# Optimization experiments

Measured on AMD Instinct MI355X. Metric: run time of the kernel, lower is better.

The kernel has to match this reference:

```python
import jax, jax.numpy as jnp
import numpy as np

DIM = 192
SCALE = DIM ** (-0.5)


def setup_inputs() -> dict:
    key = jax.random.key(0)
    qkv = jax.random.normal(key, (8, 4096, 3 * DIM), dtype=jnp.float32)
    return {"qkv": qkv}


def reference(qkv):
    # qkv: [B, T, 3C] -> q, k, v each [B, T, C]
    q, k, v = jnp.split(qkv, 3, axis=2)
    # scale_in=True: scale q and k before distance computation
    q = q * SCALE
    k = k * SCALE
    # L2-distance attention logits: -||q_t - k_s||_2, computed via the
    # expansion ||q||^2 + ||k||^2 - 2 q.k (same as torch.cdist for large inputs)
    q2 = jnp.sum(q * q, axis=-1)          # [B, T]
    k2 = jnp.sum(k * k, axis=-1)          # [B, S]
    d2 = q2[:, :, None] + k2[:, None, :] - 2.0 * jnp.einsum('btc,bsc->bts', q, k)
    d2 = jnp.maximum(d2, 0.0)
    # safe sqrt (zero distance on the diagonal since q and k come from same tokens)
    dist = jnp.where(d2 > 0, jnp.sqrt(jnp.where(d2 > 0, d2, 1.0)), 0.0)
    attn_logits = -dist                    # [B, T, S]
    attn = jax.nn.softmax(attn_logits, axis=-1)
    return jnp.einsum('bts,bsc->btc', attn, v)  # [B, T, C]
```

## Files before the change

kernel.cpp:

```cpp
#include <hip/hip_runtime.h>
#include <hip/hip_bf16.h>


#define BB 8
#define TT 4096
#define CD 192

typedef __attribute__((ext_vector_type(8))) short short8;
typedef __attribute__((ext_vector_type(4))) float float4v;
typedef __attribute__((ext_vector_type(2))) unsigned int uint2v;

constexpr float A2C = (float)(2.0813689810056077 / 192.0);

static __device__ __forceinline__ unsigned short f2bf(float f) {
  unsigned u = __builtin_bit_cast(unsigned, f);
  unsigned r = u + 0x7fffu + ((u >> 16) & 1u);
  return (unsigned short)(r >> 16);
}
static __device__ __forceinline__ float bf2f(unsigned short b) {
  return __builtin_bit_cast(float, (unsigned)b << 16);
}

__global__ __launch_bounds__(256) void prep(
    const float* __restrict__ qkv, short8* __restrict__ qsw,
    short8* __restrict__ ksw, short8* __restrict__ vsw,
    float* __restrict__ q2, float* __restrict__ k2) {
  __shared__ unsigned short tile[32 * 584];
  const int t = threadIdx.x;
  const int b = blockIdx.x >> 7;
  const int sc = blockIdx.x & 127;
  const float* src = qkv + ((size_t)(b * TT + sc * 32)) * (3 * CD);
#pragma unroll
  for (int j = 0; j < 18; ++j) {
    int f = j * 256 + t;
    int row = f / 144, c4 = (f % 144) * 4;
    float4v x = *(const float4v*)(src + (size_t)row * 576 + c4);
    unsigned r0 = (unsigned)f2bf(x[0]) | ((unsigned)f2bf(x[1]) << 16);
    unsigned r1 = (unsigned)f2bf(x[2]) | ((unsigned)f2bf(x[3]) << 16);
    *(uint2v*)&tile[row * 584 + c4] = (uint2v){r0, r1};
  }
  __syncthreads();

  const int lane = t & 63, w = t >> 6;
  const int L = lane & 15, q = lane >> 4;
  const int which = w >> 1;
  const int s16o = w & 1;
  const int row = s16o * 16 + L;
  short8* dst = which ? ksw : qsw;
  const size_t ubase = ((size_t)(b * 256 + sc * 2 + s16o)) * 6;
  float ss = 0.f;
#pragma unroll
  for (int ch = 0; ch < 6; ++ch) {
    short8 fr = *(const short8*)&tile[row * 584 + which * CD + ch * 32 + q * 8];
#pragma unroll
    for (int j = 0; j < 8; ++j) {
      float f = bf2f((unsigned short)fr[j]);
      ss += f * f;
    }
    dst[(ubase + ch) * 64 + lane] = fr;
  }
  ss += __shfl_xor(ss, 16);
  ss += __shfl_xor(ss, 32);
  if (lane < 16)
    (which ? k2 : q2)[b * TT + sc * 32 + s16o * 16 + lane] = ss * A2C;

#pragma unroll
  for (int i = 0; i < 3; ++i) {
    int nt2 = w * 3 + i;
    short8 fr;
#pragma unroll
    for (int j = 0; j < 8; ++j)
      fr[j] = (short)tile[(q * 8 + j) * 584 + 2 * CD + nt2 * 16 + L];
    vsw[((size_t)(b * 12 + nt2) * 128 + sc) * 64 + lane] = fr;
  }
}

__global__ __launch_bounds__(256, 2) void attn2(
    const short8* __restrict__ qsw, const short8* __restrict__ ksw,
    const short8* __restrict__ vsw, const float* __restrict__ q2,
    const float* __restrict__ k2, float* __restrict__ out) {
  __shared__ __align__(16) unsigned char s_lds[49152 + 9216];
  float* ldsP = (float*)(s_lds + 49152);

  const int tid = threadIdx.x;
  const int w = tid >> 6;
  const int lane = tid & 63;
  const int L = lane & 15;
  const int q = lane >> 4;
  const int b = blockIdx.x & 7;
  const int qt = blockIdx.x >> 3;
  const int q0 = qt * 64 + w * 16;
  const size_t bT = (size_t)b * TT;

  float* pw = ldsP + w * 576;

  auto stage = [&](int itile, int buf) {
    const char* gk = (const char*)(ksw + ((size_t)(b * 256 + 2 * itile)) * 6 * 64);
#pragma unroll
    for (int j = 0; j < 3; ++j) {
      int u = w * 3 + j;
      const char* ga = gk + (u * 64 + lane) * 16;
      char* la = (char*)s_lds + buf * 12288 + u * 1024;
      __builtin_amdgcn_global_load_lds(
          (const __attribute__((address_space(1))) void*)ga,
          (__attribute__((address_space(3))) void*)la, 16, 0, 0);
    }
#pragma unroll
    for (int j = 0; j < 3; ++j) {
      int u = w * 3 + j;
      const char* ga = (const char*)vsw +
                       (((size_t)(b * 12 + u) * 128 + itile) * 64 + lane) * 16;
      char* la = (char*)s_lds + 24576 + buf * 12288 + u * 1024;
      __builtin_amdgcn_global_load_lds(
          (const __attribute__((address_space(1))) void*)ga,
          (__attribute__((address_space(3))) void*)la, 16, 0, 0);
    }
  };

  short8 qf[6];
#pragma unroll
  for (int ch = 0; ch < 6; ++ch)
    qf[ch] = qsw[((size_t)(b * 256 + (q0 >> 4)) * 6 + ch) * 64 + lane];

  float q2l[4];
#pragma unroll
  for (int r = 0; r < 4; ++r) q2l[r] = q2[bT + q0 + 4 * q + r];

  float4v oacc[12];
#pragma unroll
  for (int nt = 0; nt < 12; ++nt) oacc[nt] = (float4v){0.f, 0.f, 0.f, 0.f};
  float lsum[4] = {0.f, 0.f, 0.f, 0.f};

  stage(0, 0);
  __syncthreads();

#pragma unroll 1
  for (int it = 0; it < 128; ++it) {
    const int cur = it & 1;
    if (it + 1 < 128) stage(it + 1, cur ^ 1);
    const int s0 = it * 32;

    float k2l[2];
    k2l[0] = k2[bT + s0 + L];
    k2l[1] = k2[bT + s0 + 16 + L];

    float4v sacc[2];
    sacc[0] = (float4v){0.f, 0.f, 0.f, 0.f};
    sacc[1] = (float4v){0.f, 0.f, 0.f, 0.f};
#pragma unroll
    for (int ch = 0; ch < 6; ++ch) {
      short8 kf0 = *(const short8*)(s_lds + cur * 12288 + ch * 1024 + lane * 16);
      short8 kf1 = *(const short8*)(s_lds + cur * 12288 + (6 + ch) * 1024 + lane * 16);
      sacc[0] = __builtin_amdgcn_mfma_f32_16x16x32_bf16(qf[ch], kf0, sacc[0], 0, 0, 0);
      sacc[1] = __builtin_amdgcn_mfma_f32_16x16x32_bf16(qf[ch], kf1, sacc[1], 0, 0, 0);
    }

    short8 vf[12];
#pragma unroll
    for (int nt = 0; nt < 12; ++nt)
      vf[nt] = *(const short8*)(s_lds + 24576 + cur * 12288 + nt * 1024 + lane * 16);

#pragma unroll
    for (int nt = 0; nt < 2; ++nt)
#pragma unroll
      for (int r = 0; r < 4; ++r) {
        float dot = sacc[nt][r];
        float tt = fmaf(-2.f * A2C, dot, q2l[r] + k2l[nt]);
        float y = fmaxf(tt, 0.f);
        float p = __builtin_amdgcn_exp2f(-__builtin_amdgcn_sqrtf(y));
        lsum[r] += p;
        pw[(4 * q + r) * 36 + nt * 16 + L] = p;
      }
    float4v p0 = *(const float4v*)(pw + L * 36 + q * 8);
    float4v p1 = *(const float4v*)(pw + L * 36 + q * 8 + 4);
    short8 paf;
#pragma unroll
    for (int j = 0; j < 4; ++j) {
      paf[j] = (short)f2bf(p0[j]);
      paf[j + 4] = (short)f2bf(p1[j]);
    }

#pragma unroll
    for (int nt = 0; nt < 12; ++nt)
      oacc[nt] = __builtin_amdgcn_mfma_f32_16x16x32_bf16(paf, vf[nt], oacc[nt], 0, 0, 0);

    __syncthreads();
  }

#pragma unroll
  for (int r = 0; r < 4; ++r) {
    float ls = lsum[r];
#pragma unroll
    for (int m = 1; m < 16; m <<= 1) ls += __shfl_xor(ls, m);
    float linv = 1.f / ls;
#pragma unroll
    for (int nt = 0; nt < 12; ++nt)
      out[(bT + q0 + 4 * q + r) * CD + nt * 16 + L] = oacc[nt][r] * linv;
  }
}

extern "C" void kernel_launch(void* const* d_in, const int* in_sizes, int n_in,
                              void* d_out, int out_size, void* d_ws, size_t ws_size,
                              hipStream_t stream) {
  (void)in_sizes; (void)n_in; (void)out_size; (void)ws_size;
  const float* qkv = (const float*)d_in[0];
  float* out = (float*)d_out;

  short8* qsw = (short8*)d_ws;
  short8* ksw = qsw + (size_t)BB * 256 * 6 * 64;
  short8* vsw = ksw + (size_t)BB * 256 * 6 * 64;
  float* q2 = (float*)(vsw + (size_t)BB * 12 * 128 * 64);
  float* k2 = q2 + (size_t)BB * TT;

  prep<<<BB * 128, 256, 0, stream>>>(qkv, qsw, ksw, vsw, q2, k2);
  attn2<<<BB * 64, 256, 0, stream>>>(qsw, ksw, vsw, q2, k2, out);
}
```

Measured before the change: 244.3 us.

## Switch to fp16, compute transposed scores in registers, split output channels across blocks

Converts Q/K/V staging from bf16 to fp16. Computes S^T (K as the A operand) so each lane's probabilities already sit in the layout the PV MFMA (16x16x16 f16) expects, which removes the LDS round trip through the P scratch buffer. Each wave now handles 32 query rows but only half of the 192 output channels, with a second block covering the other half. Per-block V staging and LDS usage shrink, at the cost of computing QK^T twice across the two channel-half blocks. The move to fp16 changes precision, and values outside the fp16 range could overflow.

Measured after the change: 299.7 us. +22.6%, slower.

```diff
diff --git a/kernel.cpp b/kernel.cpp
--- a/kernel.cpp
+++ b/kernel.cpp
@@ -6,25 +6,26 @@
 #define TT 4096
 #define CD 192
 
+typedef __attribute__((ext_vector_type(8))) _Float16 half8;
+typedef __attribute__((ext_vector_type(4))) _Float16 half4;
 typedef __attribute__((ext_vector_type(8))) short short8;
 typedef __attribute__((ext_vector_type(4))) float float4v;
 typedef __attribute__((ext_vector_type(2))) unsigned int uint2v;
 
 constexpr float A2C = (float)(2.0813689810056077 / 192.0);
-
-static __device__ __forceinline__ unsigned short f2bf(float f) {
-  unsigned u = __builtin_bit_cast(unsigned, f);
-  unsigned r = u + 0x7fffu + ((u >> 16) & 1u);
-  return (unsigned short)(r >> 16);
-}
-static __device__ __forceinline__ float bf2f(unsigned short b) {
-  return __builtin_bit_cast(float, (unsigned)b << 16);
+constexpr float M2A2C = -2.0f * A2C;
+
+static __device__ __forceinline__ unsigned short f2h(float f) {
+  return __builtin_bit_cast(unsigned short, (_Float16)f);
+}
+static __device__ __forceinline__ float h2f(unsigned short u) {
+  return (float)__builtin_bit_cast(_Float16, u);
 }
 
 __global__ __launch_bounds__(256) void prep(
     const float* __restrict__ qkv, short8* __restrict__ qsw,
     short8* __restrict__ ksw, short8* __restrict__ vsw,
-    float* __restrict__ q2, float* __restrict__ k2) {
+    float* __restrict__ q2A, float* __restrict__ k2A) {
   __shared__ unsigned short tile[32 * 584];
   const int t = threadIdx.x;
   const int b = blockIdx.x >> 7;
@@ -35,8 +36,8 @@
     int f = j * 256 + t;
     int row = f / 144, c4 = (f % 144) * 4;
     float4v x = *(const float4v*)(src + (size_t)row * 576 + c4);
-    unsigned r0 = (unsigned)f2bf(x[0]) | ((unsigned)f2bf(x[1]) << 16);
-    unsigned r1 = (unsigned)f2bf(x[2]) | ((unsigned)f2bf(x[3]) << 16);
+    unsigned r0 = (unsigned)f2h(x[0]) | ((unsigned)f2h(x[1]) << 16);
+    unsigned r1 = (unsigned)f2h(x[2]) | ((unsigned)f2h(x[3]) << 16);
     *(uint2v*)&tile[row * 584 + c4] = (uint2v){r0, r1};
   }
   __syncthreads();
@@ -54,7 +55,7 @@
     short8 fr = *(const short8*)&tile[row * 584 + which * CD + ch * 32 + q * 8];
 #pragma unroll
     for (int j = 0; j < 8; ++j) {
-      float f = bf2f((unsigned short)fr[j]);
+      float f = h2f((unsigned short)fr[j]);
       ss += f * f;
     }
     dst[(ubase + ch) * 64 + lane] = fr;
@@ -62,25 +63,26 @@
   ss += __shfl_xor(ss, 16);
   ss += __shfl_xor(ss, 32);
   if (lane < 16)
-    (which ? k2 : q2)[b * TT + sc * 32 + s16o * 16 + lane] = ss * A2C;
+    (which ? k2A : q2A)[b * TT + sc * 32 + s16o * 16 + lane] = ss * A2C;
 
 #pragma unroll
   for (int i = 0; i < 3; ++i) {
-    int nt2 = w * 3 + i;
+    int ct = w * 3 + i;
     short8 fr;
 #pragma unroll
-    for (int j = 0; j < 8; ++j)
-      fr[j] = (short)tile[(q * 8 + j) * 584 + 2 * CD + nt2 * 16 + L];
-    vsw[((size_t)(b * 12 + nt2) * 128 + sc) * 64 + lane] = fr;
-  }
-}
-
-__global__ __launch_bounds__(256, 2) void attn2(
+    for (int j = 0; j < 4; ++j) {
+      fr[j]     = (short)tile[(4 * q + j) * 584 + 2 * CD + ct * 16 + L];
+      fr[j + 4] = (short)tile[(16 + 4 * q + j) * 584 + 2 * CD + ct * 16 + L];
+    }
+    vsw[((size_t)(b * 12 + ct) * 128 + sc) * 64 + lane] = fr;
+  }
+}
+
+__global__ __launch_bounds__(256, 2) void attn3(
     const short8* __restrict__ qsw, const short8* __restrict__ ksw,
-    const short8* __restrict__ vsw, const float* __restrict__ q2,
-    const float* __restrict__ k2, float* __restrict__ out) {
-  __shared__ __align__(16) unsigned char s_lds[49152 + 9216];
-  float* ldsP = (float*)(s_lds + 49152);
+    const short8* __restrict__ vsw, const float* __restrict__ q2A,
+    const float* __restrict__ k2A, float* __restrict__ out) {
+  __shared__ __align__(16) unsigned char s_lds[36864];
 
   const int tid = threadIdx.x;
   const int w = tid >> 6;
@@ -88,48 +90,53 @@
   const int L = lane & 15;
   const int q = lane >> 4;
   const int b = blockIdx.x & 7;
-  const int qt = blockIdx.x >> 3;
-  const int q0 = qt * 64 + w * 16;
+  const int h = (blockIdx.x >> 3) & 1;
+  const int qt = blockIdx.x >> 4;
+  const int q0 = qt * 128 + w * 32;
   const size_t bT = (size_t)b * TT;
 
-  float* pw = ldsP + w * 576;
-
-  auto stage = [&](int itile, int buf) {
-    const char* gk = (const char*)(ksw + ((size_t)(b * 256 + 2 * itile)) * 6 * 64);
-#pragma unroll
-    for (int j = 0; j < 3; ++j) {
-      int u = w * 3 + j;
-      const char* ga = gk + (u * 64 + lane) * 16;
-      char* la = (char*)s_lds + buf * 12288 + u * 1024;
-      __builtin_amdgcn_global_load_lds(
-          (const __attribute__((address_space(1))) void*)ga,
-          (__attribute__((address_space(3))) void*)la, 16, 0, 0);
-    }
-#pragma unroll
-    for (int j = 0; j < 3; ++j) {
-      int u = w * 3 + j;
-      const char* ga = (const char*)vsw +
-                       (((size_t)(b * 12 + u) * 128 + itile) * 64 + lane) * 16;
-      char* la = (char*)s_lds + 24576 + buf * 12288 + u * 1024;
-      __builtin_amdgcn_global_load_lds(
-          (const __attribute__((address_space(1))) void*)ga,
-          (__attribute__((address_space(3))) void*)la, 16, 0, 0);
+  auto stage = [&](int it, int buf) {
+#pragma unroll
+    for (int j = 0; j < 5; ++j) {
+      int u = w + 4 * j;
+      if (u < 12) {
+        int so = u / 6, ch = u % 6;
+        const char* ga = (const char*)ksw +
+            (((size_t)(b * 256 + it * 2 + so) * 6 + ch) * 64 + lane) * 16;
+        char* la = (char*)s_lds + buf * 12288 + u * 1024;
+        __builtin_amdgcn_global_load_lds(
+            (const __attribute__((address_space(1))) void*)ga,
+            (__attribute__((address_space(3))) void*)la, 16, 0, 0);
+      } else if (u < 18) {
+        int j2 = u - 12;
+        const char* ga = (const char*)vsw +
+            (((size_t)(b * 12 + h * 6 + j2) * 128 + it) * 64 + lane) * 16;
+        char* la = (char*)s_lds + 24576 + buf * 6144 + j2 * 1024;
+        __builtin_amdgcn_global_load_lds(
+            (const __attribute__((address_space(1))) void*)ga,
+            (__attribute__((address_space(3))) void*)la, 16, 0, 0);
+      }
     }
   };
 
-  short8 qf[6];
-#pragma unroll
-  for (int ch = 0; ch < 6; ++ch)
-    qf[ch] = qsw[((size_t)(b * 256 + (q0 >> 4)) * 6 + ch) * 64 + lane];
-
-  float q2l[4];
-#pragma unroll
-  for (int r = 0; r < 4; ++r) q2l[r] = q2[bT + q0 + 4 * q + r];
-
-  float4v oacc[12];
-#pragma unroll
-  for (int nt = 0; nt < 12; ++nt) oacc[nt] = (float4v){0.f, 0.f, 0.f, 0.f};
-  float lsum[4] = {0.f, 0.f, 0.f, 0.f};
+  half8 qf[2][6];
+#pragma unroll
+  for (int mt = 0; mt < 2; ++mt)
+#pragma unroll
+    for (int ch = 0; ch < 6; ++ch)
+      qf[mt][ch] = __builtin_bit_cast(
+          half8, qsw[((size_t)(b * 256 + (q0 >> 4) + mt) * 6 + ch) * 64 + lane]);
+
+  float q2l[2];
+  q2l[0] = q2A[bT + q0 + L];
+  q2l[1] = q2A[bT + q0 + 16 + L];
+
+  float4v oacc[2][6];
+#pragma unroll
+  for (int mt = 0; mt < 2; ++mt)
+#pragma unroll
+    for (int ct = 0; ct < 6; ++ct) oacc[mt][ct] = (float4v){0.f, 0.f, 0.f, 0.f};
+  float lsum[2] = {0.f, 0.f};
 
   stage(0, 0);
   __syncthreads();
@@ -140,62 +147,69 @@
     if (it + 1 < 128) stage(it + 1, cur ^ 1);
     const int s0 = it * 32;
 
-    float k2l[2];
-    k2l[0] = k2[bT + s0 + L];
-    k2l[1] = k2[bT + s0 + 16 + L];
-
-    float4v sacc[2];
-    sacc[0] = (float4v){0.f, 0.f, 0.f, 0.f};
-    sacc[1] = (float4v){0.f, 0.f, 0.f, 0.f};
+    float4v k2l[2];
+    k2l[0] = *(const float4v*)(k2A + bT + s0 + 4 * q);
+    k2l[1] = *(const float4v*)(k2A + bT + s0 + 16 + 4 * q);
+
+    float4v sacc[2][2];
+#pragma unroll
+    for (int mt = 0; mt < 2; ++mt)
+#pragma unroll
+      for (int n = 0; n < 2; ++n) sacc[mt][n] = (float4v){0.f, 0.f, 0.f, 0.f};
 #pragma unroll
     for (int ch = 0; ch < 6; ++ch) {
-      short8 kf0 = *(const short8*)(s_lds + cur * 12288 + ch * 1024 + lane * 16);
-      short8 kf1 = *(const short8*)(s_lds + cur * 12288 + (6 + ch) * 1024 + lane * 16);
-      sacc[0] = __builtin_amdgcn_mfma_f32_16x16x32_bf16(qf[ch], kf0, sacc[0], 0, 0, 0);
-      sacc[1] = __builtin_amdgcn_mfma_f32_16x16x32_bf16(qf[ch], kf1, sacc[1], 0, 0, 0);
-    }
-
-    short8 vf[12];
-#pragma unroll
-    for (int nt = 0; nt < 12; ++nt)
-      vf[nt] = *(const short8*)(s_lds + 24576 + cur * 12288 + nt * 1024 + lane * 16);
-
-#pragma unroll
-    for (int nt = 0; nt < 2; ++nt)
-#pragma unroll
-      for (int r = 0; r < 4; ++r) {
-        float dot = sacc[nt][r];
-        float tt = fmaf(-2.f * A2C, dot, q2l[r] + k2l[nt]);
-        float y = fmaxf(tt, 0.f);
-        float p = __builtin_amdgcn_exp2f(-__builtin_amdgcn_sqrtf(y));
-        lsum[r] += p;
-        pw[(4 * q + r) * 36 + nt * 16 + L] = p;
+      half8 kf0 = *(const half8*)(s_lds + cur * 12288 + ch * 1024 + lane * 16);
+      half8 kf1 = *(const half8*)(s_lds + cur * 12288 + (6 + ch) * 1024 + lane * 16);
+      sacc[0][0] = __builtin_amdgcn_mfma_f32_16x16x32_f16(kf0, qf[0][ch], sacc[0][0], 0, 0, 0);
+      sacc[0][1] = __builtin_amdgcn_mfma_f32_16x16x32_f16(kf1, qf[0][ch], sacc[0][1], 0, 0, 0);
+      sacc[1][0] = __builtin_amdgcn_mfma_f32_16x16x32_f16(kf0, qf[1][ch], sacc[1][0], 0, 0, 0);
+      sacc[1][1] = __builtin_amdgcn_mfma_f32_16x16x32_f16(kf1, qf[1][ch], sacc[1][1], 0, 0, 0);
+    }
+
+    half4 paf[2][2];
+#pragma unroll
+    for (int mt = 0; mt < 2; ++mt)
+#pragma unroll
+      for (int n = 0; n < 2; ++n) {
+        float4v pv;
+#pragma unroll
+        for (int r = 0; r < 4; ++r) {
+          float tt = fmaf(sacc[mt][n][r], M2A2C, q2l[mt] + k2l[n][r]);
+          float p = __builtin_amdgcn_exp2f(-__builtin_amdgcn_sqrtf(fmaxf(tt, 0.f)));
+          lsum[mt] += p;
+          pv[r] = p;
+        }
+        paf[mt][n] = (half4){(_Float16)pv[0], (_Float16)pv[1],
+                             (_Float16)pv[2], (_Float16)pv[3]};
       }
-    float4v p0 = *(const float4v*)(pw + L * 36 + q * 8);
-    float4v p1 = *(const float4v*)(pw + L * 36 + q * 8 + 4);
-    short8 paf;
-#pragma unroll
-    for (int j = 0; j < 4; ++j) {
-      paf[j] = (short)f2bf(p0[j]);
-      paf[j + 4] = (short)f2bf(p1[j]);
-    }
-
-#pragma unroll
-    for (int nt = 0; nt < 12; ++nt)
-      oacc[nt] = __builtin_amdgcn_mfma_f32_16x16x32_bf16(paf, vf[nt], oacc[nt], 0, 0, 0);
+
+#pragma unroll
+    for (int ct = 0; ct < 6; ++ct) {
+      half8 vv = *(const half8*)(s_lds + 24576 + cur * 6144 + ct * 1024 + lane * 16);
+      half4 vlo = __builtin_shufflevector(vv, vv, 0, 1, 2, 3);
+      half4 vhi = __builtin_shufflevector(vv, vv, 4, 5, 6, 7);
+      oacc[0][ct] = __builtin_amdgcn_mfma_f32_16x16x16f16(paf[0][0], vlo, oacc[0][ct], 0, 0, 0);
+      oacc[0][ct] = __builtin_amdgcn_mfma_f32_16x16x16f16(paf[0][1], vhi, oacc[0][ct], 0, 0, 0);
+      oacc[1][ct] = __builtin_amdgcn_mfma_f32_16x16x16f16(paf[1][0], vlo, oacc[1][ct], 0, 0, 0);
+      oacc[1][ct] = __builtin_amdgcn_mfma_f32_16x16x16f16(paf[1][1], vhi, oacc[1][ct], 0, 0, 0);
+    }
 
     __syncthreads();
   }
 
 #pragma unroll
-  for (int r = 0; r < 4; ++r) {
-    float ls = lsum[r];
-#pragma unroll
-    for (int m = 1; m < 16; m <<= 1) ls += __shfl_xor(ls, m);
-    float linv = 1.f / ls;
-#pragma unroll
-    for (int nt = 0; nt < 12; ++nt)
-      out[(bT + q0 + 4 * q + r) * CD + nt * 16 + L] = oacc[nt][r] * linv;
+  for (int mt = 0; mt < 2; ++mt) {
+    float ls = lsum[mt];
+    ls += __shfl_xor(ls, 16);
+    ls += __shfl_xor(ls, 32);
+#pragma unroll
+    for (int r = 0; r < 4; ++r) {
+      float linv = 1.f / __shfl(ls, 4 * q + r);
+#pragma unroll
+      for (int ct = 0; ct < 6; ++ct)
+        out[(bT + q0 + mt * 16 + 4 * q + r) * CD + (h * 6 + ct) * 16 + L] =
+            oacc[mt][ct][r] * linv;
+    }
   }
 }
 
@@ -209,9 +223,9 @@
   short8* qsw = (short8*)d_ws;
   short8* ksw = qsw + (size_t)BB * 256 * 6 * 64;
   short8* vsw = ksw + (size_t)BB * 256 * 6 * 64;
-  float* q2 = (float*)(vsw + (size_t)BB * 12 * 128 * 64);
-  float* k2 = q2 + (size_t)BB * TT;
-
-  prep<<<BB * 128, 256, 0, stream>>>(qkv, qsw, ksw, vsw, q2, k2);
-  attn2<<<BB * 64, 256, 0, stream>>>(qsw, ksw, vsw, q2, k2, out);
-}
+  float* q2A = (float*)(vsw + (size_t)BB * 12 * 128 * 64);
+  float* k2A = q2A + (size_t)BB * TT;
+
+  prep<<<BB * 128, 256, 0, stream>>>(qkv, qsw, ksw, vsw, q2A, k2A);
+  attn3<<<BB * 64, 256, 0, stream>>>(qsw, ksw, vsw, q2A, k2A, out);
+}
```
